# Kernel tuning notes

Measured on AMD Instinct MI355X. Metric: run time of the kernel, lower is better.

Reference implementation:

```python
import jax, jax.numpy as jnp
import numpy as np

N_STATES, N_OBS = 64, 32
N_TRAJ, T = 128, 250
ALPHA, BETA, KAPPA = 1.0, 2.0, -1.0
DT = 0.02
LAM = ALPHA ** 2 * (N_STATES + KAPPA) - N_STATES  # Merwe scaling lambda


def _weights(n):
    c = 0.5 / (n + LAM)
    Wm = jnp.full((2 * n + 1,), c, dtype=jnp.float32).at[0].set(LAM / (n + LAM))
    Wc = Wm.at[0].add(1.0 - ALPHA ** 2 + BETA)
    return Wm, Wc


def setup_inputs() -> dict:
    key = jax.random.key(0)
    k1, k2, k3, k4 = jax.random.split(key, 4)
    X = jax.random.normal(k1, (N_TRAJ, T, N_STATES), jnp.float32)
    Y = jax.random.normal(k2, (N_TRAJ, T, N_OBS), jnp.float32)
    F = jax.random.normal(k3, (N_STATES, N_STATES), jnp.float32) / np.sqrt(N_STATES)
    H = jax.random.normal(k4, (N_OBS, N_STATES), jnp.float32) / np.sqrt(N_STATES)
    Q = 0.01 * jnp.eye(N_STATES, dtype=jnp.float32)   # q2 * I, as in ctor
    R = 0.01 * jnp.eye(N_OBS, dtype=jnp.float32)      # r2 * I, as in ctor
    return {"X": X, "Y": Y, "F": F, "H": H, "Q": Q, "R": R}


def _sigma_points(x, P):
    # MerweScaledSigmaPoints: rows of upper-triangular chol((n+lam)P) == cols of lower chol
    n = x.shape[0]
    L = jnp.linalg.cholesky((n + LAM) * (P + 1e-8 * jnp.eye(n, dtype=P.dtype)))
    offs = L.T  # (n, n): row i is the i-th sigma offset
    return jnp.concatenate([x[None], x[None] + offs, x[None] - offs], axis=0)  # (2n+1, n)


def _ukf_step(carry, y, F, H, Q, R, Wm, Wc):
    x, P = carry
    # predict: propagate sigma points through fx(x, dt) = x + dt * tanh(F @ x)
    sig = _sigma_points(x, P)                 # (2n+1, n)
    sf = sig + DT * jnp.tanh(sig @ F.T)       # (2n+1, n)
    x_pred = Wm @ sf
    dxs = sf - x_pred
    P_pred = jnp.einsum('k,ki,kj->ij', Wc, dxs, dxs) + Q
    # update: hx(x) = H @ x applied to predicted sigma points (filterpy reuses sigmas_f)
    zs = sf @ H.T                             # (2n+1, m)
    z_pred = Wm @ zs
    dzs = zs - z_pred
    Pz = jnp.einsum('k,ki,kj->ij', Wc, dzs, dzs) + R
    Pxz = jnp.einsum('k,ki,kj->ij', Wc, dxs, dzs)
    K = jnp.linalg.solve(Pz, Pxz.T).T         # Pxz @ inv(Pz)
    x_new = x_pred + K @ (y - z_pred)
    P_new = P_pred - K @ Pz @ K.T
    P_new = 0.5 * (P_new + P_new.T)
    return (x_new, P_new), (x_new, P_new)


def reference(X, Y, F, H, Q, R):
    n = F.shape[0]
    Wm, Wc = _weights(n)

    def run_one(y_seq):
        x0 = jnp.zeros((n,), dtype=Y.dtype)             # ukf.x = zeros
        P0 = 1e-5 * jnp.eye(n, dtype=Y.dtype)           # ukf.P = 1e-5 * I
        step = lambda c, y: _ukf_step(c, y, F, H, Q, R, Wm, Wc)
        _, (xs, Ps) = jax.lax.scan(step, (x0, P0), y_seq)
        return xs, Ps

    traj_estimated, Pk_estimated = jax.vmap(run_one)(Y)  # (N,T,n), (N,T,n,n)
    mse_lin = jnp.mean((traj_estimated - X) ** 2, axis=(1, 2))  # per-traj MSE
    mse_lin_avg = jnp.mean(mse_lin)
    mse_db_avg = 10.0 * jnp.log10(mse_lin_avg)
    return traj_estimated, Pk_estimated, mse_lin_avg, mse_db_avg
```

## Files before the change

### kernel.cpp

```cpp
#include <hip/hip_runtime.h>
#include <math.h>


#define NTRAJ 128
#define TSTEPS 250
#define NS 64
#define NO 32
#define PS 65
#define SFS 68
#define HTS 36
#define PXS 33
#define GJS 65
#define BLK 256

#define DTc 0.02f
#define W_C (0.5f/63.0f)
#define WM0 (-1.0f/63.0f)
#define WC0 (2.0f - 1.0f/63.0f)

__device__ __forceinline__ float tanh_fast(float x) {
  float e = __expf(2.0f * x);
  return 1.0f - 2.0f / (e + 1.0f);
}

__global__ __launch_bounds__(BLK)
void ukf_main(const float* __restrict__ Xg, const float* __restrict__ Yg,
              const float* __restrict__ Fg, const float* __restrict__ Hg,
              const float* __restrict__ Qg, const float* __restrict__ Rg,
              float* __restrict__ outX, float* __restrict__ outP,
              float* __restrict__ wsPart)
{
  __shared__ __align__(16) float P[NS*PS];
  __shared__ __align__(16) float sfb[128*SFS];
  __shared__ __align__(16) float sHT[NS*HTS];
  __shared__ float sPart[4*NS];
  __shared__ float sx[NS], sxp[NS], sFx[NS], s0[NS];
  __shared__ float sinn[NO];

  float* Pxz = sfb;
  float* Km  = sfb + NS*PXS;
  float* Wgj = sfb + 2*NS*PXS;
  float* Mb  = sfb + 2*NS*PXS;

  const int tid  = threadIdx.x;
  const int lane = tid & 63;
  const int grp  = tid >> 6;
  const int traj = blockIdx.x;

  for (int o = tid; o < NS*NS; o += BLK) {
    int i = o >> 6, j = o & 63;
    P[i*PS + j] = (i == j) ? 1e-5f : 0.f;
  }
  for (int o = tid; o < NO*NS; o += BLK) {
    int m = o >> 6, j = o & 63;
    sHT[j*HTS + m] = Hg[o];
  }
  if (tid < NS) sx[tid] = 0.f;
  float errAcc = 0.f;
  __syncthreads();

  for (int t = 0; t < TSTEPS; ++t) {
    const size_t sbase = (size_t)traj*TSTEPS + t;

    for (int o = tid; o < NS*NS; o += BLK) {
      int i = o >> 6, j = o & 63;
      float v = P[i*PS + j] * 63.f;
      if (i == j) v += 6.3e-7f;
      P[i*PS + j] = v;
      sfb[j*SFS + i] = Fg[o];
    }
    __syncthreads();

    for (int pc = 0; pc < NS; pc += 8) {
      if (grp == 0) {
        const int i = lane;
        float pr[8];
        #pragma unroll
        for (int jj = 0; jj < 8; ++jj) pr[jj] = P[i*PS + pc + jj];
        #pragma unroll
        for (int jj = 0; jj < 8; ++jj) {
          const int gc = pc + jj;
          float dv  = __shfl(pr[jj], gc);
          float inv = rsqrtf(dv);
          float d   = dv * inv;
          pr[jj] = (i == gc) ? d : pr[jj] * inv;
          #pragma unroll
          for (int kk = jj + 1; kk < 8; ++kk) {
            float ck = __shfl(pr[jj], pc + kk);
            pr[kk] = fmaf(-pr[jj], ck, pr[kk]);
          }
        }
        #pragma unroll
        for (int jj = 0; jj < 8; ++jj) P[i*PS + pc + jj] = pr[jj];
      }
      __syncthreads();
      if (pc < NS - 8) {
        const int i = lane;
        float Li[8];
        #pragma unroll
        for (int jj = 0; jj < 8; ++jj) Li[jj] = P[i*PS + pc + jj];
        for (int k = pc + 8 + grp; k < NS; k += 4) {
          float acc = P[i*PS + k];
          #pragma unroll
          for (int jj = 0; jj < 8; ++jj)
            acc = fmaf(-Li[jj], P[k*PS + pc + jj], acc);
          P[i*PS + k] = acc;
        }
        __syncthreads();
      }
    }

    {
      const int c0 = (tid >> 4) << 2;
      const int j0 = (tid & 15) << 2;
      float acc[4][4];
      #pragma unroll
      for (int a = 0; a < 4; ++a)
        #pragma unroll
        for (int b = 0; b < 4; ++b) acc[a][b] = 0.f;
      for (int jj = 0; jj < NS; ++jj) {
        float4 fv = *(const float4*)&sfb[jj*SFS + j0];
        float lv[4];
        #pragma unroll
        for (int a = 0; a < 4; ++a) {
          int cc = c0 + a;
          lv[a] = (jj >= cc) ? P[jj*PS + cc] : 0.f;
        }
        #pragma unroll
        for (int a = 0; a < 4; ++a) {
          acc[a][0] = fmaf(lv[a], fv.x, acc[a][0]);
          acc[a][1] = fmaf(lv[a], fv.y, acc[a][1]);
          acc[a][2] = fmaf(lv[a], fv.z, acc[a][2]);
          acc[a][3] = fmaf(lv[a], fv.w, acc[a][3]);
        }
      }
      #pragma unroll
      for (int a = 0; a < 4; ++a) {
        float4 w4; w4.x = acc[a][0]; w4.y = acc[a][1]; w4.z = acc[a][2]; w4.w = acc[a][3];
        *(float4*)&sfb[(64 + c0 + a)*SFS + j0] = w4;
      }
    }
    if (tid < NS) {
      float a2 = 0.f;
      for (int jj = 0; jj < NS; ++jj) a2 = fmaf(sfb[jj*SFS + tid], sx[jj], a2);
      sFx[tid] = a2;
    }
    __syncthreads();

    {
      const int j = lane;
      float psum = 0.f;
      float xv = sx[j], fxv = sFx[j];
      for (int cc = grp; cc < NS; cc += 4) {
        float flv = sfb[(64+cc)*SFS + j];
        float Lv  = (j >= cc) ? P[j*PS + cc] : 0.f;
        float vp = xv + Lv + DTc * tanh_fast(fxv + flv);
        float vm = xv - Lv + DTc * tanh_fast(fxv - flv);
        sfb[cc*SFS + j]      = vp;
        sfb[(64+cc)*SFS + j] = vm;
        psum += vp + vm;
      }
      sPart[grp*NS + j] = psum;
    }
    if (tid < NS) s0[tid] = sx[tid] + DTc * tanh_fast(sFx[tid]);
    __syncthreads();

    if (tid < NS) {
      float xp = fmaf(W_C, sPart[tid] + sPart[NS+tid] + sPart[2*NS+tid] + sPart[3*NS+tid],
                      WM0 * s0[tid]);
      sxp[tid] = xp;
      s0[tid] -= xp;
    }
    __syncthreads();

    {
      const int i0 = (tid >> 4) << 2;
      const int j0 = (tid & 15) << 2;
      float acc[4][4];
      #pragma unroll
      for (int a = 0; a < 4; ++a)
        #pragma unroll
        for (int b = 0; b < 4; ++b) acc[a][b] = 0.f;
      float xi[4], xj[4];
      #pragma unroll
      for (int a = 0; a < 4; ++a) { xi[a] = sxp[i0+a]; xj[a] = sxp[j0+a]; }
      for (int r = 0; r < 128; ++r) {
        float4 av = *(const float4*)&sfb[r*SFS + i0];
        float4 bv = *(const float4*)&sfb[r*SFS + j0];
        float da[4] = {av.x - xi[0], av.y - xi[1], av.z - xi[2], av.w - xi[3]};
        float db[4] = {bv.x - xj[0], bv.y - xj[1], bv.z - xj[2], bv.w - xj[3]};
        #pragma unroll
        for (int a = 0; a < 4; ++a)
          #pragma unroll
          for (int b = 0; b < 4; ++b) acc[a][b] = fmaf(da[a], db[b], acc[a][b]);
      }
      const int rot = (i0 >> 2) & 3;
      #pragma unroll
      for (int a = 0; a < 4; ++a) {
        float d0a = s0[i0+a];
        #pragma unroll
        for (int b = 0; b < 4; ++b) {
          int bb = (b + rot) & 3;
          P[(i0+a)*PS + j0 + bb] = fmaf(WC0 * d0a, s0[j0+bb], W_C * acc[a][bb]);
        }
      }
    }
    __syncthreads();

    {
      const int i = lane;
      const int cb = grp * 8;
      float acc[8];
      #pragma unroll
      for (int u = 0; u < 8; ++u) acc[u] = 0.f;
      for (int jj = 0; jj < NS; ++jj) {
        float pv = P[i*PS + jj];
        float4 h0 = *(const float4*)&sHT[jj*HTS + cb];
        float4 h1 = *(const float4*)&sHT[jj*HTS + cb + 4];
        acc[0] = fmaf(pv, h0.x, acc[0]); acc[1] = fmaf(pv, h0.y, acc[1]);
        acc[2] = fmaf(pv, h0.z, acc[2]); acc[3] = fmaf(pv, h0.w, acc[3]);
        acc[4] = fmaf(pv, h1.x, acc[4]); acc[5] = fmaf(pv, h1.y, acc[5]);
        acc[6] = fmaf(pv, h1.z, acc[6]); acc[7] = fmaf(pv, h1.w, acc[7]);
      }
      #pragma unroll
      for (int u = 0; u < 8; ++u) Pxz[i*PXS + cb + u] = acc[u];
    }
    __syncthreads();

    {
      const int m = tid >> 3;
      const int n0 = tid & 7;
      float acc[4];
      #pragma unroll
      for (int q = 0; q < 4; ++q) acc[q] = Rg[m*NO + n0 + 8*q];
      for (int i2 = 0; i2 < NS; ++i2) {
        float hv = sHT[i2*HTS + m];
        #pragma unroll
        for (int q = 0; q < 4; ++q)
          acc[q] = fmaf(hv, Pxz[i2*PXS + n0 + 8*q], acc[q]);
      }
      #pragma unroll
      for (int q = 0; q < 4; ++q) Wgj[m*GJS + n0 + 8*q] = acc[q];
    }
    __syncthreads();

    if (grp == 0) {
      const int c = lane;
      float w[NO];
      #pragma unroll
      for (int r = 0; r < NO; ++r)
        w[r] = (c < NO) ? Wgj[r*GJS + c] : ((c - NO == r) ? 1.f : 0.f);
      #pragma unroll
      for (int p = 0; p < NO; ++p) {
        float piv = __shfl(w[p], p);
        float rp  = 1.0f / piv;
        float wp  = w[p] * rp;
        #pragma unroll
        for (int r = 0; r < NO; ++r) {
          if (r == p) continue;
          float cr = __shfl(w[r], p);
          w[r] = fmaf(-cr, wp, w[r]);
        }
        w[p] = wp;
      }
      if (c >= NO) {
        #pragma unroll
        for (int r = 0; r < NO; ++r) Wgj[(c - NO)*PXS + r] = w[r];
      }
    } else if (grp == 1) {
      if (lane < NO) {
        float z = 0.f;
        for (int jj = 0; jj < NS; ++jj) z = fmaf(sHT[jj*HTS + lane], sxp[jj], z);
        sinn[lane] = Yg[sbase*NO + lane] - z;
      }
    } else {
      for (int o = tid - 128; o < NS*NS; o += 128) {
        int i = o >> 6, j = o & 63;
        P[i*PS + j] += Qg[o];
      }
    }
    __syncthreads();

    {
      const int i = lane;
      const int cb = grp * 8;
      float acc[8];
      #pragma unroll
      for (int u = 0; u < 8; ++u) acc[u] = 0.f;
      for (int n2 = 0; n2 < NO; ++n2) {
        float pv = Pxz[i*PXS + n2];
        #pragma unroll
        for (int u = 0; u < 8; ++u)
          acc[u] = fmaf(pv, Wgj[(cb + u)*PXS + n2], acc[u]);
      }
      #pragma unroll
      for (int u = 0; u < 8; ++u) Km[i*PXS + cb + u] = acc[u];
    }
    __syncthreads();

    if (tid < 136) {
      int r = (int)((sqrtf(8.f*(float)tid + 1.f) - 1.f) * 0.5f);
      while ((r+1)*(r+2)/2 <= tid) ++r;
      while (r*(r+1)/2 > tid) --r;
      const int c2 = tid - ((r*(r+1)) >> 1);
      const int i0 = r << 2, j0 = c2 << 2;
      float acc[4][4];
      #pragma unroll
      for (int a = 0; a < 4; ++a)
        #pragma unroll
        for (int b = 0; b < 4; ++b) acc[a][b] = 0.f;
      for (int m = 0; m < NO; ++m) {
        float ka[4], pb[4];
        #pragma unroll
        for (int a = 0; a < 4; ++a) ka[a] = Km[(i0+a)*PXS + m];
        #pragma unroll
        for (int b = 0; b < 4; ++b) pb[b] = Pxz[(j0+b)*PXS + m];
        #pragma unroll
        for (int a = 0; a < 4; ++a)
          #pragma unroll
          for (int b = 0; b < 4; ++b) acc[a][b] = fmaf(ka[a], pb[b], acc[a][b]);
      }
      #pragma unroll
      for (int a = 0; a < 4; ++a)
        #pragma unroll
        for (int b = 0; b < 4; ++b) Mb[(i0+a)*GJS + j0 + b] = acc[a][b];
    } else if (tid >= 192) {
      const int i = tid - 192;
      float xn = sxp[i];
      #pragma unroll 8
      for (int m = 0; m < NO; ++m) xn = fmaf(Km[i*PXS + m], sinn[m], xn);
      sx[i] = xn;
      outX[sbase*NS + i] = xn;
      float dd = xn - Xg[sbase*NS + i];
      errAcc = fmaf(dd, dd, errAcc);
    }
    __syncthreads();

    for (int o = tid; o < NS*NS; o += BLK) {
      int i = o >> 6, j = o & 63;
      float mv = (i >= j) ? Mb[i*GJS + j] : Mb[j*GJS + i];
      float v = P[i*PS + j] - mv;
      P[i*PS + j] = v;
      outP[sbase*(size_t)(NS*NS) + o] = v;
    }
    __syncthreads();
  }

  sPart[tid] = errAcc;
  __syncthreads();
  if (tid < 64) {
    float v = sPart[tid] + sPart[tid+64] + sPart[tid+128] + sPart[tid+192];
    for (int off = 32; off > 0; off >>= 1) v += __shfl_down(v, off);
    if (tid == 0) wsPart[traj] = v;
  }
}

__global__ __launch_bounds__(128)
void mse_reduce(const float* __restrict__ part, float* __restrict__ outS)
{
  __shared__ float sbuf[128];
  int tid = threadIdx.x;
  sbuf[tid] = part[tid];
  __syncthreads();
  if (tid < 64) {
    float v = sbuf[tid] + sbuf[tid + 64];
    for (int off = 32; off > 0; off >>= 1) v += __shfl_down(v, off);
    if (tid == 0) {
      float m = v / (128.f * 250.f * 64.f);
      outS[0] = m;
      outS[1] = 10.f * log10f(m);
    }
  }
}

extern "C" void kernel_launch(void* const* d_in, const int* in_sizes, int n_in,
                              void* d_out, int out_size, void* d_ws, size_t ws_size,
                              hipStream_t stream) {
  const float* Xg = (const float*)d_in[0];
  const float* Yg = (const float*)d_in[1];
  const float* Fg = (const float*)d_in[2];
  const float* Hg = (const float*)d_in[3];
  const float* Qg = (const float*)d_in[4];
  const float* Rg = (const float*)d_in[5];

  float* outX = (float*)d_out;
  float* outP = outX + (size_t)NTRAJ*TSTEPS*NS;
  float* outS = outP + (size_t)NTRAJ*TSTEPS*NS*NS;
  float* wsP  = (float*)d_ws;

  hipLaunchKernelGGL(ukf_main, dim3(NTRAJ), dim3(BLK), 0, stream,
                     Xg, Yg, Fg, Hg, Qg, Rg, outX, outP, wsP);
  hipLaunchKernelGGL(mse_reduce, dim3(1), dim3(128), 0, stream, wsP, outS);
}
```

Before: 11.76 ms.

## Double block size to 512 threads and rebalance per-step work partitions

Raises the block from 256 to 512 threads and re-partitions every per-timestep stage (Cholesky trailing update, L·F product, covariance outer product, Pxz, Pz, gain, K·Pxzᵀ) so each thread owns a smaller tile. It also widens the Cholesky panel from 8 to 16 columns to cut barriers, and folds the 63x scale plus jitter into the end-of-step P write so one full pass and one sync disappear. The F transpose load now overlaps the first panel factorization, and R is preloaded into registers. The price is more threads per block competing for registers with 16-wide panel arrays, and lower per-thread ILP in the small GEMMs.

Result: faster. 9.780 ms (-16.8%).

```diff
diff --git a/kernel.cpp b/kernel.cpp
--- a/kernel.cpp
+++ b/kernel.cpp
@@ -11,7 +11,7 @@
 #define HTS 36
 #define PXS 33
 #define GJS 65
-#define BLK 256
+#define BLK 512
 
 #define DTc 0.02f
 #define W_C (0.5f/63.0f)
@@ -33,7 +33,7 @@
   __shared__ __align__(16) float P[NS*PS];
   __shared__ __align__(16) float sfb[128*SFS];
   __shared__ __align__(16) float sHT[NS*HTS];
-  __shared__ float sPart[4*NS];
+  __shared__ float sPart[8*NS];
   __shared__ float sx[NS], sxp[NS], sFx[NS], s0[NS];
   __shared__ float sinn[NO];
 
@@ -47,9 +47,14 @@
   const int grp  = tid >> 6;
   const int traj = blockIdx.x;
 
+  const int pzm = tid >> 4;
+  const int pzn = tid & 15;
+  const float rv0 = Rg[pzm*NO + pzn];
+  const float rv1 = Rg[pzm*NO + pzn + 16];
+
   for (int o = tid; o < NS*NS; o += BLK) {
     int i = o >> 6, j = o & 63;
-    P[i*PS + j] = (i == j) ? 1e-5f : 0.f;
+    P[i*PS + j] = (i == j) ? (63e-5f + 6.3e-7f) : 0.f;
   }
   for (int o = tid; o < NO*NS; o += BLK) {
     int m = o >> 6, j = o & 63;
@@ -62,47 +67,42 @@
   for (int t = 0; t < TSTEPS; ++t) {
     const size_t sbase = (size_t)traj*TSTEPS + t;
 
-    for (int o = tid; o < NS*NS; o += BLK) {
-      int i = o >> 6, j = o & 63;
-      float v = P[i*PS + j] * 63.f;
-      if (i == j) v += 6.3e-7f;
-      P[i*PS + j] = v;
-      sfb[j*SFS + i] = Fg[o];
-    }
-    __syncthreads();
-
-    for (int pc = 0; pc < NS; pc += 8) {
+    for (int pc = 0; pc < NS; pc += 16) {
       if (grp == 0) {
         const int i = lane;
-        float pr[8];
-        #pragma unroll
-        for (int jj = 0; jj < 8; ++jj) pr[jj] = P[i*PS + pc + jj];
-        #pragma unroll
-        for (int jj = 0; jj < 8; ++jj) {
+        float pr[16];
+        #pragma unroll
+        for (int jj = 0; jj < 16; ++jj) pr[jj] = P[i*PS + pc + jj];
+        #pragma unroll
+        for (int jj = 0; jj < 16; ++jj) {
           const int gc = pc + jj;
           float dv  = __shfl(pr[jj], gc);
           float inv = rsqrtf(dv);
-          float d   = dv * inv;
-          pr[jj] = (i == gc) ? d : pr[jj] * inv;
+          pr[jj] = (i == gc) ? dv * inv : pr[jj] * inv;
           #pragma unroll
-          for (int kk = jj + 1; kk < 8; ++kk) {
+          for (int kk = jj + 1; kk < 16; ++kk) {
             float ck = __shfl(pr[jj], pc + kk);
             pr[kk] = fmaf(-pr[jj], ck, pr[kk]);
           }
         }
         #pragma unroll
-        for (int jj = 0; jj < 8; ++jj) P[i*PS + pc + jj] = pr[jj];
+        for (int jj = 0; jj < 16; ++jj) P[i*PS + pc + jj] = pr[jj];
+      } else if (pc == 0) {
+        for (int o = tid - 64; o < NS*NS; o += (BLK - 64)) {
+          int i = o >> 6, j = o & 63;
+          sfb[j*SFS + i] = Fg[o];
+        }
       }
       __syncthreads();
-      if (pc < NS - 8) {
+      if (pc < NS - 16) {
         const int i = lane;
-        float Li[8];
-        #pragma unroll
-        for (int jj = 0; jj < 8; ++jj) Li[jj] = P[i*PS + pc + jj];
-        for (int k = pc + 8 + grp; k < NS; k += 4) {
+        float Li[16];
+        #pragma unroll
+        for (int jj = 0; jj < 16; ++jj) Li[jj] = P[i*PS + pc + jj];
+        for (int k = pc + 16 + grp; k < NS; k += 8) {
           float acc = P[i*PS + k];
           #pragma unroll
-          for (int jj = 0; jj < 8; ++jj)
+          for (int jj = 0; jj < 16; ++jj)
             acc = fmaf(-Li[jj], P[k*PS + pc + jj], acc);
           P[i*PS + k] = acc;
         }
@@ -111,34 +111,23 @@
     }
 
     {
-      const int c0 = (tid >> 4) << 2;
+      const int c0 = (tid >> 4) << 1;
       const int j0 = (tid & 15) << 2;
-      float acc[4][4];
-      #pragma unroll
-      for (int a = 0; a < 4; ++a)
-        #pragma unroll
-        for (int b = 0; b < 4; ++b) acc[a][b] = 0.f;
+      float a00=0.f,a01=0.f,a02=0.f,a03=0.f, a10=0.f,a11=0.f,a12=0.f,a13=0.f;
+      #pragma unroll 2
       for (int jj = 0; jj < NS; ++jj) {
         float4 fv = *(const float4*)&sfb[jj*SFS + j0];
-        float lv[4];
-        #pragma unroll
-        for (int a = 0; a < 4; ++a) {
-          int cc = c0 + a;
-          lv[a] = (jj >= cc) ? P[jj*PS + cc] : 0.f;
-        }
-        #pragma unroll
-        for (int a = 0; a < 4; ++a) {
-          acc[a][0] = fmaf(lv[a], fv.x, acc[a][0]);
-          acc[a][1] = fmaf(lv[a], fv.y, acc[a][1]);
-          acc[a][2] = fmaf(lv[a], fv.z, acc[a][2]);
-          acc[a][3] = fmaf(lv[a], fv.w, acc[a][3]);
-        }
-      }
-      #pragma unroll
-      for (int a = 0; a < 4; ++a) {
-        float4 w4; w4.x = acc[a][0]; w4.y = acc[a][1]; w4.z = acc[a][2]; w4.w = acc[a][3];
-        *(float4*)&sfb[(64 + c0 + a)*SFS + j0] = w4;
-      }
+        float lv0 = (jj >= c0)     ? P[jj*PS + c0]     : 0.f;
+        float lv1 = (jj >= c0 + 1) ? P[jj*PS + c0 + 1] : 0.f;
+        a00 = fmaf(lv0, fv.x, a00); a01 = fmaf(lv0, fv.y, a01);
+        a02 = fmaf(lv0, fv.z, a02); a03 = fmaf(lv0, fv.w, a03);
+        a10 = fmaf(lv1, fv.x, a10); a11 = fmaf(lv1, fv.y, a11);
+        a12 = fmaf(lv1, fv.z, a12); a13 = fmaf(lv1, fv.w, a13);
+      }
+      float4 w0; w0.x=a00; w0.y=a01; w0.z=a02; w0.w=a03;
+      float4 w1; w1.x=a10; w1.y=a11; w1.z=a12; w1.w=a13;
+      *(float4*)&sfb[(64 + c0)*SFS + j0]     = w0;
+      *(float4*)&sfb[(64 + c0 + 1)*SFS + j0] = w1;
     }
     if (tid < NS) {
       float a2 = 0.f;
@@ -151,7 +140,7 @@
       const int j = lane;
       float psum = 0.f;
       float xv = sx[j], fxv = sFx[j];
-      for (int cc = grp; cc < NS; cc += 4) {
+      for (int cc = grp; cc < NS; cc += 8) {
         float flv = sfb[(64+cc)*SFS + j];
         float Lv  = (j >= cc) ? P[j*PS + cc] : 0.f;
         float vp = xv + Lv + DTc * tanh_fast(fxv + flv);
@@ -166,81 +155,72 @@
     __syncthreads();
 
     if (tid < NS) {
-      float xp = fmaf(W_C, sPart[tid] + sPart[NS+tid] + sPart[2*NS+tid] + sPart[3*NS+tid],
-                      WM0 * s0[tid]);
+      float s = sPart[tid]        + sPart[NS+tid]   + sPart[2*NS+tid] + sPart[3*NS+tid]
+              + sPart[4*NS+tid]   + sPart[5*NS+tid] + sPart[6*NS+tid] + sPart[7*NS+tid];
+      float xp = fmaf(W_C, s, WM0 * s0[tid]);
       sxp[tid] = xp;
       s0[tid] -= xp;
     }
     __syncthreads();
 
     {
-      const int i0 = (tid >> 4) << 2;
-      const int j0 = (tid & 15) << 2;
-      float acc[4][4];
-      #pragma unroll
-      for (int a = 0; a < 4; ++a)
-        #pragma unroll
-        for (int b = 0; b < 4; ++b) acc[a][b] = 0.f;
-      float xi[4], xj[4];
-      #pragma unroll
-      for (int a = 0; a < 4; ++a) { xi[a] = sxp[i0+a]; xj[a] = sxp[j0+a]; }
+      const int i0 = (tid >> 5) << 2;
+      const int j0 = (tid & 31) << 1;
+      float acc[4][2];
+      #pragma unroll
+      for (int a = 0; a < 4; ++a) { acc[a][0] = 0.f; acc[a][1] = 0.f; }
+      float xi[4];
+      #pragma unroll
+      for (int a = 0; a < 4; ++a) xi[a] = sxp[i0+a];
+      const float xj0 = sxp[j0], xj1 = sxp[j0+1];
+      #pragma unroll 4
       for (int r = 0; r < 128; ++r) {
         float4 av = *(const float4*)&sfb[r*SFS + i0];
-        float4 bv = *(const float4*)&sfb[r*SFS + j0];
-        float da[4] = {av.x - xi[0], av.y - xi[1], av.z - xi[2], av.w - xi[3]};
-        float db[4] = {bv.x - xj[0], bv.y - xj[1], bv.z - xj[2], bv.w - xj[3]};
-        #pragma unroll
-        for (int a = 0; a < 4; ++a)
-          #pragma unroll
-          for (int b = 0; b < 4; ++b) acc[a][b] = fmaf(da[a], db[b], acc[a][b]);
-      }
-      const int rot = (i0 >> 2) & 3;
+        float2 bv = *(const float2*)&sfb[r*SFS + j0];
+        float db0 = bv.x - xj0, db1 = bv.y - xj1;
+        #pragma unroll
+        for (int a = 0; a < 4; ++a) {
+          float da = ((const float*)&av)[a] - xi[a];
+          acc[a][0] = fmaf(da, db0, acc[a][0]);
+          acc[a][1] = fmaf(da, db1, acc[a][1]);
+        }
+      }
+      const float d0j0 = s0[j0], d0j1 = s0[j0+1];
       #pragma unroll
       for (int a = 0; a < 4; ++a) {
-        float d0a = s0[i0+a];
-        #pragma unroll
-        for (int b = 0; b < 4; ++b) {
-          int bb = (b + rot) & 3;
-          P[(i0+a)*PS + j0 + bb] = fmaf(WC0 * d0a, s0[j0+bb], W_C * acc[a][bb]);
-        }
+        float d0a = WC0 * s0[i0+a];
+        P[(i0+a)*PS + j0]     = fmaf(d0a, d0j0, W_C * acc[a][0]);
+        P[(i0+a)*PS + j0 + 1] = fmaf(d0a, d0j1, W_C * acc[a][1]);
       }
     }
     __syncthreads();
 
     {
       const int i = lane;
-      const int cb = grp * 8;
-      float acc[8];
-      #pragma unroll
-      for (int u = 0; u < 8; ++u) acc[u] = 0.f;
+      const int cb = grp * 4;
+      float acc0=0.f, acc1=0.f, acc2=0.f, acc3=0.f;
       for (int jj = 0; jj < NS; ++jj) {
         float pv = P[i*PS + jj];
-        float4 h0 = *(const float4*)&sHT[jj*HTS + cb];
-        float4 h1 = *(const float4*)&sHT[jj*HTS + cb + 4];
-        acc[0] = fmaf(pv, h0.x, acc[0]); acc[1] = fmaf(pv, h0.y, acc[1]);
-        acc[2] = fmaf(pv, h0.z, acc[2]); acc[3] = fmaf(pv, h0.w, acc[3]);
-        acc[4] = fmaf(pv, h1.x, acc[4]); acc[5] = fmaf(pv, h1.y, acc[5]);
-        acc[6] = fmaf(pv, h1.z, acc[6]); acc[7] = fmaf(pv, h1.w, acc[7]);
-      }
-      #pragma unroll
-      for (int u = 0; u < 8; ++u) Pxz[i*PXS + cb + u] = acc[u];
-    }
-    __syncthreads();
-
-    {
-      const int m = tid >> 3;
-      const int n0 = tid & 7;
-      float acc[4];
-      #pragma unroll
-      for (int q = 0; q < 4; ++q) acc[q] = Rg[m*NO + n0 + 8*q];
+        float4 h = *(const float4*)&sHT[jj*HTS + cb];
+        acc0 = fmaf(pv, h.x, acc0); acc1 = fmaf(pv, h.y, acc1);
+        acc2 = fmaf(pv, h.z, acc2); acc3 = fmaf(pv, h.w, acc3);
+      }
+      Pxz[i*PXS + cb]     = acc0;
+      Pxz[i*PXS + cb + 1] = acc1;
+      Pxz[i*PXS + cb + 2] = acc2;
+      Pxz[i*PXS + cb + 3] = acc3;
+    }
+    __syncthreads();
+
+    {
+      float a0 = rv0, a1 = rv1;
       for (int i2 = 0; i2 < NS; ++i2) {
-        float hv = sHT[i2*HTS + m];
-        #pragma unroll
-        for (int q = 0; q < 4; ++q)
-          acc[q] = fmaf(hv, Pxz[i2*PXS + n0 + 8*q], acc[q]);
-      }
-      #pragma unroll
-      for (int q = 0; q < 4; ++q) Wgj[m*GJS + n0 + 8*q] = acc[q];
+        float hv = sHT[i2*HTS + pzm];
+        a0 = fmaf(hv, Pxz[i2*PXS + pzn], a0);
+        a1 = fmaf(hv, Pxz[i2*PXS + pzn + 16], a1);
+      }
+      Wgj[pzm*GJS + pzn]      = a0;
+      Wgj[pzm*GJS + pzn + 16] = a1;
     }
     __syncthreads();
 
@@ -274,7 +254,7 @@
         sinn[lane] = Yg[sbase*NO + lane] - z;
       }
     } else {
-      for (int o = tid - 128; o < NS*NS; o += 128) {
+      for (int o = tid - 128; o < NS*NS; o += 6*64) {
         int i = o >> 6, j = o & 63;
         P[i*PS + j] += Qg[o];
       }
@@ -283,49 +263,50 @@
 
     {
       const int i = lane;
-      const int cb = grp * 8;
-      float acc[8];
-      #pragma unroll
-      for (int u = 0; u < 8; ++u) acc[u] = 0.f;
+      const int cb = grp * 4;
+      float acc0=0.f, acc1=0.f, acc2=0.f, acc3=0.f;
       for (int n2 = 0; n2 < NO; ++n2) {
         float pv = Pxz[i*PXS + n2];
-        #pragma unroll
-        for (int u = 0; u < 8; ++u)
-          acc[u] = fmaf(pv, Wgj[(cb + u)*PXS + n2], acc[u]);
-      }
-      #pragma unroll
-      for (int u = 0; u < 8; ++u) Km[i*PXS + cb + u] = acc[u];
-    }
-    __syncthreads();
-
-    if (tid < 136) {
-      int r = (int)((sqrtf(8.f*(float)tid + 1.f) - 1.f) * 0.5f);
-      while ((r+1)*(r+2)/2 <= tid) ++r;
-      while (r*(r+1)/2 > tid) --r;
-      const int c2 = tid - ((r*(r+1)) >> 1);
-      const int i0 = r << 2, j0 = c2 << 2;
-      float acc[4][4];
-      #pragma unroll
-      for (int a = 0; a < 4; ++a)
-        #pragma unroll
-        for (int b = 0; b < 4; ++b) acc[a][b] = 0.f;
+        acc0 = fmaf(pv, Wgj[(cb    )*PXS + n2], acc0);
+        acc1 = fmaf(pv, Wgj[(cb + 1)*PXS + n2], acc1);
+        acc2 = fmaf(pv, Wgj[(cb + 2)*PXS + n2], acc2);
+        acc3 = fmaf(pv, Wgj[(cb + 3)*PXS + n2], acc3);
+      }
+      Km[i*PXS + cb]     = acc0;
+      Km[i*PXS + cb + 1] = acc1;
+      Km[i*PXS + cb + 2] = acc2;
+      Km[i*PXS + cb + 3] = acc3;
+    }
+    __syncthreads();
+
+    if (tid < 272) {
+      int k = (int)((sqrtf(4.f*(float)tid + 1.f) - 1.f) * 0.5f);
+      while ((k+1)*(k+2) <= tid) ++k;
+      while (k*(k+1) > tid) --k;
+      const int r0 = tid - k*(k+1);
+      const int rb  = (r0 <= k) ? (2*k) : (2*k + 1);
+      const int cb2 = (r0 <= k) ? r0 : (r0 - (k + 1));
+      const int i0 = rb << 1, j0 = cb2 << 2;
+      float acc[2][4];
+      #pragma unroll
+      for (int b = 0; b < 4; ++b) { acc[0][b] = 0.f; acc[1][b] = 0.f; }
       for (int m = 0; m < NO; ++m) {
-        float ka[4], pb[4];
-        #pragma unroll
-        for (int a = 0; a < 4; ++a) ka[a] = Km[(i0+a)*PXS + m];
-        #pragma unroll
-        for (int b = 0; b < 4; ++b) pb[b] = Pxz[(j0+b)*PXS + m];
-        #pragma unroll
-        for (int a = 0; a < 4; ++a)
-          #pragma unroll
-          for (int b = 0; b < 4; ++b) acc[a][b] = fmaf(ka[a], pb[b], acc[a][b]);
-      }
-      #pragma unroll
-      for (int a = 0; a < 4; ++a)
-        #pragma unroll
-        for (int b = 0; b < 4; ++b) Mb[(i0+a)*GJS + j0 + b] = acc[a][b];
-    } else if (tid >= 192) {
-      const int i = tid - 192;
+        float ka0 = Km[i0*PXS + m];
+        float ka1 = Km[(i0+1)*PXS + m];
+        #pragma unroll
+        for (int b = 0; b < 4; ++b) {
+          float pb = Pxz[(j0+b)*PXS + m];
+          acc[0][b] = fmaf(ka0, pb, acc[0][b]);
+          acc[1][b] = fmaf(ka1, pb, acc[1][b]);
+        }
+      }
+      #pragma unroll
+      for (int b = 0; b < 4; ++b) {
+        Mb[i0*GJS + j0 + b]     = acc[0][b];
+        Mb[(i0+1)*GJS + j0 + b] = acc[1][b];
+      }
+    } else if (tid >= 448) {
+      const int i = tid - 448;
       float xn = sxp[i];
       #pragma unroll 8
       for (int m = 0; m < NO; ++m) xn = fmaf(Km[i*PXS + m], sinn[m], xn);
@@ -340,18 +321,18 @@
       int i = o >> 6, j = o & 63;
       float mv = (i >= j) ? Mb[i*GJS + j] : Mb[j*GJS + i];
       float v = P[i*PS + j] - mv;
-      P[i*PS + j] = v;
       outP[sbase*(size_t)(NS*NS) + o] = v;
-    }
-    __syncthreads();
-  }
-
-  sPart[tid] = errAcc;
-  __syncthreads();
-  if (tid < 64) {
-    float v = sPart[tid] + sPart[tid+64] + sPart[tid+128] + sPart[tid+192];
+      float nv = v * 63.f;
+      if (i == j) nv += 6.3e-7f;
+      P[i*PS + j] = nv;
+    }
+    __syncthreads();
+  }
+
+  if (grp == 7) {
+    float v = errAcc;
     for (int off = 32; off > 0; off >>= 1) v += __shfl_down(v, off);
-    if (tid == 0) wsPart[traj] = v;
+    if (lane == 0) wsPart[traj] = v;
   }
 }
 
```

## Restructure UKF step: blocked Cholesky, HP-based gain, fused covariance update

Applied to the files above, without the earlier changes.

Doubles the block to 512 threads and makes the Cholesky use 32-column panels, which cuts the number of barriers per step. The cross-covariance is rewritten as T = H·P_pred so that Pz = T·Hᵀ + R and K = Tᵀ·Pz⁻¹, and the rank update K·T is fused with the +Q, the output write and the next step's 63x scaling plus jitter. Redundant elementwise passes, index recomputation and scalar shared loads are removed in favour of float4 tiles, and the sigma-point mean is subtracted once in place. The costs are more register pressure from the 32-wide panel and new algebraic paths, which could change numerics slightly. Work is also imbalanced across the larger block.

After: 11.19 ms. 4.8% less time.

```diff
diff --git a/kernel.cpp b/kernel.cpp
--- a/kernel.cpp
+++ b/kernel.cpp
@@ -6,17 +6,20 @@
 #define TSTEPS 250
 #define NS 64
 #define NO 32
-#define PS 65
+#define PS 68
 #define SFS 68
 #define HTS 36
-#define PXS 33
-#define GJS 65
-#define BLK 256
+#define TS 68
+#define GJS 68
+#define PZS 36
+#define KS 36
+#define BLK 512
 
 #define DTc 0.02f
 #define W_C (0.5f/63.0f)
 #define WM0 (-1.0f/63.0f)
 #define WC0 (2.0f - 1.0f/63.0f)
+#define DEPS 6.3e-7f
 
 __device__ __forceinline__ float tanh_fast(float x) {
   float e = __expf(2.0f * x);
@@ -33,14 +36,17 @@
   __shared__ __align__(16) float P[NS*PS];
   __shared__ __align__(16) float sfb[128*SFS];
   __shared__ __align__(16) float sHT[NS*HTS];
-  __shared__ float sPart[4*NS];
-  __shared__ float sx[NS], sxp[NS], sFx[NS], s0[NS];
-  __shared__ float sinn[NO];
-
-  float* Pxz = sfb;
-  float* Km  = sfb + NS*PXS;
-  float* Wgj = sfb + 2*NS*PXS;
-  float* Mb  = sfb + 2*NS*PXS;
+  __shared__ __align__(16) float sPart[8*NS];
+  __shared__ __align__(16) float sx[NS];
+  __shared__ __align__(16) float sxp[NS];
+  __shared__ __align__(16) float sFx[NS];
+  __shared__ __align__(16) float s0[NS];
+  __shared__ __align__(16) float sinn[NO];
+
+  float* Tb  = sfb;
+  float* Pzb = sfb + 2176;
+  float* Pzi = sfb + 4352;
+  float* Km  = sfb + 5504;
 
   const int tid  = threadIdx.x;
   const int lane = tid & 63;
@@ -49,7 +55,7 @@
 
   for (int o = tid; o < NS*NS; o += BLK) {
     int i = o >> 6, j = o & 63;
-    P[i*PS + j] = (i == j) ? 1e-5f : 0.f;
+    P[i*PS + j] = (i == j) ? (63e-5f + DEPS) : 0.f;
   }
   for (int o = tid; o < NO*NS; o += BLK) {
     int m = o >> 6, j = o & 63;
@@ -62,55 +68,65 @@
   for (int t = 0; t < TSTEPS; ++t) {
     const size_t sbase = (size_t)traj*TSTEPS + t;
 
-    for (int o = tid; o < NS*NS; o += BLK) {
-      int i = o >> 6, j = o & 63;
-      float v = P[i*PS + j] * 63.f;
-      if (i == j) v += 6.3e-7f;
-      P[i*PS + j] = v;
-      sfb[j*SFS + i] = Fg[o];
-    }
-    __syncthreads();
-
-    for (int pc = 0; pc < NS; pc += 8) {
+    for (int pc = 0; pc < NS; pc += 32) {
       if (grp == 0) {
         const int i = lane;
-        float pr[8];
-        #pragma unroll
-        for (int jj = 0; jj < 8; ++jj) pr[jj] = P[i*PS + pc + jj];
-        #pragma unroll
-        for (int jj = 0; jj < 8; ++jj) {
+        float pr[32];
+        #pragma unroll
+        for (int c4 = 0; c4 < 8; ++c4)
+          *(float4*)&pr[c4*4] = *(const float4*)&P[i*PS + pc + c4*4];
+        #pragma unroll
+        for (int jj = 0; jj < 32; ++jj) {
           const int gc = pc + jj;
           float dv  = __shfl(pr[jj], gc);
           float inv = rsqrtf(dv);
-          float d   = dv * inv;
-          pr[jj] = (i == gc) ? d : pr[jj] * inv;
-          #pragma unroll
-          for (int kk = jj + 1; kk < 8; ++kk) {
+          pr[jj] = (i == gc) ? dv * inv : ((i < gc) ? 0.f : pr[jj] * inv);
+          #pragma unroll
+          for (int kk = jj + 1; kk < 32; ++kk) {
             float ck = __shfl(pr[jj], pc + kk);
             pr[kk] = fmaf(-pr[jj], ck, pr[kk]);
           }
         }
         #pragma unroll
-        for (int jj = 0; jj < 8; ++jj) P[i*PS + pc + jj] = pr[jj];
+        for (int c4 = 0; c4 < 8; ++c4)
+          *(float4*)&P[i*PS + pc + c4*4] = *(const float4*)&pr[c4*4];
+      } else if (pc == 0) {
+        for (int c = tid - 64; c < 1024; c += (BLK - 64)) {
+          int i = c >> 4, j0 = (c & 15) << 2;
+          float4 fv = *(const float4*)&Fg[i*64 + j0];
+          sfb[(j0    )*SFS + i] = fv.x;
+          sfb[(j0 + 1)*SFS + i] = fv.y;
+          sfb[(j0 + 2)*SFS + i] = fv.z;
+          sfb[(j0 + 3)*SFS + i] = fv.w;
+        }
       }
       __syncthreads();
-      if (pc < NS - 8) {
-        const int i = lane;
-        float Li[8];
-        #pragma unroll
-        for (int jj = 0; jj < 8; ++jj) Li[jj] = P[i*PS + pc + jj];
-        for (int k = pc + 8 + grp; k < NS; k += 4) {
+      if (pc == 0) {
+        const int k  = 32 + (lane & 31);
+        const int ib = 32 + grp*2 + (lane >> 5);
+        float Lk[32];
+        #pragma unroll
+        for (int c4 = 0; c4 < 8; ++c4)
+          *(float4*)&Lk[c4*4] = *(const float4*)&P[k*PS + c4*4];
+        #pragma unroll
+        for (int it = 0; it < 2; ++it) {
+          const int i = ib + 16*it;
           float acc = P[i*PS + k];
           #pragma unroll
-          for (int jj = 0; jj < 8; ++jj)
-            acc = fmaf(-Li[jj], P[k*PS + pc + jj], acc);
+          for (int c4 = 0; c4 < 8; ++c4) {
+            float4 pi = *(const float4*)&P[i*PS + c4*4];
+            acc = fmaf(-pi.x, Lk[c4*4    ], acc);
+            acc = fmaf(-pi.y, Lk[c4*4 + 1], acc);
+            acc = fmaf(-pi.z, Lk[c4*4 + 2], acc);
+            acc = fmaf(-pi.w, Lk[c4*4 + 3], acc);
+          }
           P[i*PS + k] = acc;
         }
         __syncthreads();
       }
     }
 
-    {
+    if (tid < 256) {
       const int c0 = (tid >> 4) << 2;
       const int j0 = (tid & 15) << 2;
       float acc[4][4];
@@ -120,30 +136,25 @@
         for (int b = 0; b < 4; ++b) acc[a][b] = 0.f;
       for (int jj = 0; jj < NS; ++jj) {
         float4 fv = *(const float4*)&sfb[jj*SFS + j0];
-        float lv[4];
-        #pragma unroll
-        for (int a = 0; a < 4; ++a) {
-          int cc = c0 + a;
-          lv[a] = (jj >= cc) ? P[jj*PS + cc] : 0.f;
-        }
-        #pragma unroll
-        for (int a = 0; a < 4; ++a) {
-          acc[a][0] = fmaf(lv[a], fv.x, acc[a][0]);
-          acc[a][1] = fmaf(lv[a], fv.y, acc[a][1]);
-          acc[a][2] = fmaf(lv[a], fv.z, acc[a][2]);
-          acc[a][3] = fmaf(lv[a], fv.w, acc[a][3]);
-        }
-      }
-      #pragma unroll
-      for (int a = 0; a < 4; ++a) {
-        float4 w4; w4.x = acc[a][0]; w4.y = acc[a][1]; w4.z = acc[a][2]; w4.w = acc[a][3];
-        *(float4*)&sfb[(64 + c0 + a)*SFS + j0] = w4;
-      }
-    }
-    if (tid < NS) {
+        float4 lv = *(const float4*)&P[jj*PS + c0];
+        float fa[4] = {fv.x, fv.y, fv.z, fv.w};
+        float lb[4] = {lv.x, lv.y, lv.z, lv.w};
+        #pragma unroll
+        for (int a = 0; a < 4; ++a)
+          #pragma unroll
+          for (int b = 0; b < 4; ++b)
+            acc[a][b] = fmaf(lb[b], fa[a], acc[a][b]);
+      }
+      #pragma unroll
+      for (int b = 0; b < 4; ++b) {
+        float4 w4; w4.x = acc[0][b]; w4.y = acc[1][b]; w4.z = acc[2][b]; w4.w = acc[3][b];
+        *(float4*)&sfb[(64 + c0 + b)*SFS + j0] = w4;
+      }
+    } else if (grp == 4) {
+      const int i2 = lane;
       float a2 = 0.f;
-      for (int jj = 0; jj < NS; ++jj) a2 = fmaf(sfb[jj*SFS + tid], sx[jj], a2);
-      sFx[tid] = a2;
+      for (int jj = 0; jj < NS; ++jj) a2 = fmaf(sfb[jj*SFS + i2], sx[jj], a2);
+      sFx[i2] = a2;
     }
     __syncthreads();
 
@@ -151,13 +162,13 @@
       const int j = lane;
       float psum = 0.f;
       float xv = sx[j], fxv = sFx[j];
-      for (int cc = grp; cc < NS; cc += 4) {
-        float flv = sfb[(64+cc)*SFS + j];
-        float Lv  = (j >= cc) ? P[j*PS + cc] : 0.f;
+      for (int cc = grp; cc < NS; cc += 8) {
+        float flv = sfb[(64 + cc)*SFS + j];
+        float Lv  = P[j*PS + cc];
         float vp = xv + Lv + DTc * tanh_fast(fxv + flv);
         float vm = xv - Lv + DTc * tanh_fast(fxv - flv);
-        sfb[cc*SFS + j]      = vp;
-        sfb[(64+cc)*SFS + j] = vm;
+        sfb[cc*SFS + j]        = vp;
+        sfb[(64 + cc)*SFS + j] = vm;
         psum += vp + vm;
       }
       sPart[grp*NS + j] = psum;
@@ -166,14 +177,28 @@
     __syncthreads();
 
     if (tid < NS) {
-      float xp = fmaf(W_C, sPart[tid] + sPart[NS+tid] + sPart[2*NS+tid] + sPart[3*NS+tid],
-                      WM0 * s0[tid]);
+      float s = sPart[tid]        + sPart[NS+tid]   + sPart[2*NS+tid] + sPart[3*NS+tid]
+              + sPart[4*NS+tid]   + sPart[5*NS+tid] + sPart[6*NS+tid] + sPart[7*NS+tid];
+      float xp = fmaf(W_C, s, WM0 * s0[tid]);
       sxp[tid] = xp;
       s0[tid] -= xp;
     }
     __syncthreads();
 
     {
+      const int j0 = (tid & 15) << 2;
+      float4 xp4 = *(const float4*)&sxp[j0];
+      #pragma unroll
+      for (int q = 0; q < 4; ++q) {
+        const int r = (tid >> 4) + (q << 5);
+        float4 v = *(const float4*)&sfb[r*SFS + j0];
+        v.x -= xp4.x; v.y -= xp4.y; v.z -= xp4.z; v.w -= xp4.w;
+        *(float4*)&sfb[r*SFS + j0] = v;
+      }
+    }
+    __syncthreads();
+
+    if (tid < 256) {
       const int i0 = (tid >> 4) << 2;
       const int j0 = (tid & 15) << 2;
       float acc[4][4];
@@ -181,66 +206,99 @@
       for (int a = 0; a < 4; ++a)
         #pragma unroll
         for (int b = 0; b < 4; ++b) acc[a][b] = 0.f;
-      float xi[4], xj[4];
-      #pragma unroll
-      for (int a = 0; a < 4; ++a) { xi[a] = sxp[i0+a]; xj[a] = sxp[j0+a]; }
+      #pragma unroll 4
       for (int r = 0; r < 128; ++r) {
         float4 av = *(const float4*)&sfb[r*SFS + i0];
         float4 bv = *(const float4*)&sfb[r*SFS + j0];
-        float da[4] = {av.x - xi[0], av.y - xi[1], av.z - xi[2], av.w - xi[3]};
-        float db[4] = {bv.x - xj[0], bv.y - xj[1], bv.z - xj[2], bv.w - xj[3]};
+        float da[4] = {av.x, av.y, av.z, av.w};
+        float db[4] = {bv.x, bv.y, bv.z, bv.w};
         #pragma unroll
         for (int a = 0; a < 4; ++a)
           #pragma unroll
-          for (int b = 0; b < 4; ++b) acc[a][b] = fmaf(da[a], db[b], acc[a][b]);
-      }
-      const int rot = (i0 >> 2) & 3;
+          for (int b = 0; b < 4; ++b)
+            acc[a][b] = fmaf(da[a], db[b], acc[a][b]);
+      }
+      float4 si = *(const float4*)&s0[i0];
+      float4 sj = *(const float4*)&s0[j0];
+      float s0i[4] = {si.x, si.y, si.z, si.w};
+      float s0j[4] = {sj.x, sj.y, sj.z, sj.w};
       #pragma unroll
       for (int a = 0; a < 4; ++a) {
-        float d0a = s0[i0+a];
-        #pragma unroll
-        for (int b = 0; b < 4; ++b) {
-          int bb = (b + rot) & 3;
-          P[(i0+a)*PS + j0 + bb] = fmaf(WC0 * d0a, s0[j0+bb], W_C * acc[a][bb]);
-        }
-      }
-    }
-    __syncthreads();
-
-    {
-      const int i = lane;
-      const int cb = grp * 8;
-      float acc[8];
-      #pragma unroll
-      for (int u = 0; u < 8; ++u) acc[u] = 0.f;
-      for (int jj = 0; jj < NS; ++jj) {
-        float pv = P[i*PS + jj];
-        float4 h0 = *(const float4*)&sHT[jj*HTS + cb];
-        float4 h1 = *(const float4*)&sHT[jj*HTS + cb + 4];
-        acc[0] = fmaf(pv, h0.x, acc[0]); acc[1] = fmaf(pv, h0.y, acc[1]);
-        acc[2] = fmaf(pv, h0.z, acc[2]); acc[3] = fmaf(pv, h0.w, acc[3]);
-        acc[4] = fmaf(pv, h1.x, acc[4]); acc[5] = fmaf(pv, h1.y, acc[5]);
-        acc[6] = fmaf(pv, h1.z, acc[6]); acc[7] = fmaf(pv, h1.w, acc[7]);
-      }
-      #pragma unroll
-      for (int u = 0; u < 8; ++u) Pxz[i*PXS + cb + u] = acc[u];
-    }
-    __syncthreads();
-
-    {
-      const int m = tid >> 3;
-      const int n0 = tid & 7;
-      float acc[4];
-      #pragma unroll
-      for (int q = 0; q < 4; ++q) acc[q] = Rg[m*NO + n0 + 8*q];
-      for (int i2 = 0; i2 < NS; ++i2) {
-        float hv = sHT[i2*HTS + m];
-        #pragma unroll
-        for (int q = 0; q < 4; ++q)
-          acc[q] = fmaf(hv, Pxz[i2*PXS + n0 + 8*q], acc[q]);
-      }
-      #pragma unroll
-      for (int q = 0; q < 4; ++q) Wgj[m*GJS + n0 + 8*q] = acc[q];
+        float d0a = WC0 * s0i[a];
+        float4 w4;
+        w4.x = fmaf(d0a, s0j[0], W_C * acc[a][0]);
+        w4.y = fmaf(d0a, s0j[1], W_C * acc[a][1]);
+        w4.z = fmaf(d0a, s0j[2], W_C * acc[a][2]);
+        w4.w = fmaf(d0a, s0j[3], W_C * acc[a][3]);
+        *(float4*)&P[(i0 + a)*PS + j0] = w4;
+      }
+    } else if (grp == 4) {
+      if (lane < NO) {
+        float z = 0.f;
+        for (int jj = 0; jj < NS; ++jj) z = fmaf(sHT[jj*HTS + lane], sxp[jj], z);
+        sinn[lane] = Yg[sbase*NO + lane] - z;
+      }
+    }
+    __syncthreads();
+
+    if (tid < 128) {
+      const int m0 = (tid >> 4) << 2;
+      const int c0 = (tid & 15) << 2;
+      float acc[4][4];
+      #pragma unroll
+      for (int a = 0; a < 4; ++a)
+        #pragma unroll
+        for (int b = 0; b < 4; ++b) acc[a][b] = 0.f;
+      for (int jj = 0; jj < NS; jj += 4) {
+        float hv[16], pv[16];
+        #pragma unroll
+        for (int k2 = 0; k2 < 4; ++k2) {
+          *(float4*)&hv[k2*4] = *(const float4*)&sHT[(jj + k2)*HTS + m0];
+          *(float4*)&pv[k2*4] = *(const float4*)&P[(jj + k2)*PS + c0];
+        }
+        #pragma unroll
+        for (int k2 = 0; k2 < 4; ++k2)
+          #pragma unroll
+          for (int a = 0; a < 4; ++a)
+            #pragma unroll
+            for (int b = 0; b < 4; ++b)
+              acc[a][b] = fmaf(hv[k2*4 + a], pv[k2*4 + b], acc[a][b]);
+      }
+      #pragma unroll
+      for (int a = 0; a < 4; ++a) {
+        float4 w4; w4.x = acc[a][0]; w4.y = acc[a][1]; w4.z = acc[a][2]; w4.w = acc[a][3];
+        *(float4*)&Tb[(m0 + a)*TS + c0] = w4;
+      }
+    }
+    __syncthreads();
+
+    if (tid < 128) {
+      const int m0 = (tid >> 3) << 1;
+      const int n0 = (tid & 7) << 2;
+      float4 r0 = *(const float4*)&Rg[m0*NO + n0];
+      float4 r1 = *(const float4*)&Rg[(m0 + 1)*NO + n0];
+      float acc[2][4] = {{r0.x, r0.y, r0.z, r0.w}, {r1.x, r1.y, r1.z, r1.w}};
+      for (int jj = 0; jj < NS; jj += 4) {
+        float t0[4], t1[4], hv[16];
+        *(float4*)t0 = *(const float4*)&Tb[m0*TS + jj];
+        *(float4*)t1 = *(const float4*)&Tb[(m0 + 1)*TS + jj];
+        #pragma unroll
+        for (int k2 = 0; k2 < 4; ++k2)
+          *(float4*)&hv[k2*4] = *(const float4*)&sHT[(jj + k2)*HTS + n0];
+        #pragma unroll
+        for (int k2 = 0; k2 < 4; ++k2) {
+          #pragma unroll
+          for (int b = 0; b < 4; ++b) {
+            acc[0][b] = fmaf(t0[k2], hv[k2*4 + b], acc[0][b]);
+            acc[1][b] = fmaf(t1[k2], hv[k2*4 + b], acc[1][b]);
+          }
+        }
+      }
+      #pragma unroll
+      for (int a = 0; a < 2; ++a) {
+        float4 w4; w4.x = acc[a][0]; w4.y = acc[a][1]; w4.z = acc[a][2]; w4.w = acc[a][3];
+        *(float4*)&Pzb[(m0 + a)*GJS + n0] = w4;
+      }
     }
     __syncthreads();
 
@@ -249,7 +307,7 @@
       float w[NO];
       #pragma unroll
       for (int r = 0; r < NO; ++r)
-        w[r] = (c < NO) ? Wgj[r*GJS + c] : ((c - NO == r) ? 1.f : 0.f);
+        w[r] = (c < NO) ? Pzb[r*GJS + c] : ((c - NO == r) ? 1.f : 0.f);
       #pragma unroll
       for (int p = 0; p < NO; ++p) {
         float piv = __shfl(w[p], p);
@@ -265,93 +323,127 @@
       }
       if (c >= NO) {
         #pragma unroll
-        for (int r = 0; r < NO; ++r) Wgj[(c - NO)*PXS + r] = w[r];
-      }
-    } else if (grp == 1) {
-      if (lane < NO) {
-        float z = 0.f;
-        for (int jj = 0; jj < NS; ++jj) z = fmaf(sHT[jj*HTS + lane], sxp[jj], z);
-        sinn[lane] = Yg[sbase*NO + lane] - z;
-      }
-    } else {
-      for (int o = tid - 128; o < NS*NS; o += 128) {
-        int i = o >> 6, j = o & 63;
-        P[i*PS + j] += Qg[o];
-      }
-    }
-    __syncthreads();
-
-    {
-      const int i = lane;
-      const int cb = grp * 8;
-      float acc[8];
-      #pragma unroll
-      for (int u = 0; u < 8; ++u) acc[u] = 0.f;
-      for (int n2 = 0; n2 < NO; ++n2) {
-        float pv = Pxz[i*PXS + n2];
-        #pragma unroll
-        for (int u = 0; u < 8; ++u)
-          acc[u] = fmaf(pv, Wgj[(cb + u)*PXS + n2], acc[u]);
-      }
-      #pragma unroll
-      for (int u = 0; u < 8; ++u) Km[i*PXS + cb + u] = acc[u];
+        for (int r = 0; r < NO; ++r) Pzi[(c - NO)*PZS + r] = w[r];
+      }
+    }
+    __syncthreads();
+
+    if (tid < 128) {
+      const int i0 = (tid & 15) << 2;
+      const int cb = (tid >> 4) << 2;
+      float acc[4][4];
+      #pragma unroll
+      for (int a = 0; a < 4; ++a)
+        #pragma unroll
+        for (int b = 0; b < 4; ++b) acc[a][b] = 0.f;
+      for (int n = 0; n < NO; n += 4) {
+        float tv[16], zv[16];
+        #pragma unroll
+        for (int k2 = 0; k2 < 4; ++k2)
+          *(float4*)&tv[k2*4] = *(const float4*)&Tb[(n + k2)*TS + i0];
+        #pragma unroll
+        for (int b = 0; b < 4; ++b)
+          *(float4*)&zv[b*4] = *(const float4*)&Pzi[(cb + b)*PZS + n];
+        #pragma unroll
+        for (int k2 = 0; k2 < 4; ++k2)
+          #pragma unroll
+          for (int a = 0; a < 4; ++a)
+            #pragma unroll
+            for (int b = 0; b < 4; ++b)
+              acc[a][b] = fmaf(tv[k2*4 + a], zv[b*4 + k2], acc[a][b]);
+      }
+      #pragma unroll
+      for (int a = 0; a < 4; ++a) {
+        float4 w4; w4.x = acc[a][0]; w4.y = acc[a][1]; w4.z = acc[a][2]; w4.w = acc[a][3];
+        *(float4*)&Km[(i0 + a)*KS + cb] = w4;
+      }
     }
     __syncthreads();
 
     if (tid < 136) {
       int r = (int)((sqrtf(8.f*(float)tid + 1.f) - 1.f) * 0.5f);
-      while ((r+1)*(r+2)/2 <= tid) ++r;
-      while (r*(r+1)/2 > tid) --r;
-      const int c2 = tid - ((r*(r+1)) >> 1);
+      while ((r + 1)*(r + 2)/2 <= tid) ++r;
+      while (r*(r + 1)/2 > tid) --r;
+      const int c2 = tid - ((r*(r + 1)) >> 1);
       const int i0 = r << 2, j0 = c2 << 2;
+      const bool diag = (r == c2);
       float acc[4][4];
       #pragma unroll
       for (int a = 0; a < 4; ++a)
         #pragma unroll
         for (int b = 0; b < 4; ++b) acc[a][b] = 0.f;
-      for (int m = 0; m < NO; ++m) {
-        float ka[4], pb[4];
-        #pragma unroll
-        for (int a = 0; a < 4; ++a) ka[a] = Km[(i0+a)*PXS + m];
-        #pragma unroll
-        for (int b = 0; b < 4; ++b) pb[b] = Pxz[(j0+b)*PXS + m];
+      for (int m = 0; m < NO; m += 4) {
+        float ka[16], tb[16];
         #pragma unroll
         for (int a = 0; a < 4; ++a)
-          #pragma unroll
-          for (int b = 0; b < 4; ++b) acc[a][b] = fmaf(ka[a], pb[b], acc[a][b]);
-      }
-      #pragma unroll
-      for (int a = 0; a < 4; ++a)
-        #pragma unroll
-        for (int b = 0; b < 4; ++b) Mb[(i0+a)*GJS + j0 + b] = acc[a][b];
-    } else if (tid >= 192) {
-      const int i = tid - 192;
+          *(float4*)&ka[a*4] = *(const float4*)&Km[(i0 + a)*KS + m];
+        #pragma unroll
+        for (int k2 = 0; k2 < 4; ++k2)
+          *(float4*)&tb[k2*4] = *(const float4*)&Tb[(m + k2)*TS + j0];
+        #pragma unroll
+        for (int k2 = 0; k2 < 4; ++k2)
+          #pragma unroll
+          for (int a = 0; a < 4; ++a)
+            #pragma unroll
+            for (int b = 0; b < 4; ++b)
+              acc[a][b] = fmaf(ka[a*4 + k2], tb[k2*4 + b], acc[a][b]);
+      }
+      float vres[4][4];
+      #pragma unroll
+      for (int a = 0; a < 4; ++a) {
+        float4 pv = *(const float4*)&P[(i0 + a)*PS + j0];
+        float4 qv = *(const float4*)&Qg[(i0 + a)*64 + j0];
+        float pa[4] = {pv.x + qv.x, pv.y + qv.y, pv.z + qv.z, pv.w + qv.w};
+        #pragma unroll
+        for (int b = 0; b < 4; ++b) {
+          float mv = diag ? ((a >= b) ? acc[a][b] : acc[b][a]) : acc[a][b];
+          vres[a][b] = pa[b] - mv;
+        }
+      }
+      #pragma unroll
+      for (int a = 0; a < 4; ++a) {
+        float4 g; g.x = vres[a][0]; g.y = vres[a][1]; g.z = vres[a][2]; g.w = vres[a][3];
+        *(float4*)&outP[sbase*(size_t)(NS*NS) + (i0 + a)*64 + j0] = g;
+        float4 sres;
+        sres.x = fmaf(vres[a][0], 63.f, (diag && a == 0) ? DEPS : 0.f);
+        sres.y = fmaf(vres[a][1], 63.f, (diag && a == 1) ? DEPS : 0.f);
+        sres.z = fmaf(vres[a][2], 63.f, (diag && a == 2) ? DEPS : 0.f);
+        sres.w = fmaf(vres[a][3], 63.f, (diag && a == 3) ? DEPS : 0.f);
+        *(float4*)&P[(i0 + a)*PS + j0] = sres;
+      }
+      if (!diag) {
+        #pragma unroll
+        for (int b = 0; b < 4; ++b) {
+          float4 g; g.x = vres[0][b]; g.y = vres[1][b]; g.z = vres[2][b]; g.w = vres[3][b];
+          *(float4*)&outP[sbase*(size_t)(NS*NS) + (j0 + b)*64 + i0] = g;
+          float4 s2; s2.x = g.x*63.f; s2.y = g.y*63.f; s2.z = g.z*63.f; s2.w = g.w*63.f;
+          *(float4*)&P[(j0 + b)*PS + i0] = s2;
+        }
+      }
+    } else if (tid >= 448) {
+      const int i = tid - 448;
       float xn = sxp[i];
-      #pragma unroll 8
-      for (int m = 0; m < NO; ++m) xn = fmaf(Km[i*PXS + m], sinn[m], xn);
+      #pragma unroll
+      for (int mc = 0; mc < NO; mc += 4) {
+        float4 kv = *(const float4*)&Km[i*KS + mc];
+        float4 iv = *(const float4*)&sinn[mc];
+        xn = fmaf(kv.x, iv.x, xn);
+        xn = fmaf(kv.y, iv.y, xn);
+        xn = fmaf(kv.z, iv.z, xn);
+        xn = fmaf(kv.w, iv.w, xn);
+      }
       sx[i] = xn;
       outX[sbase*NS + i] = xn;
       float dd = xn - Xg[sbase*NS + i];
       errAcc = fmaf(dd, dd, errAcc);
     }
     __syncthreads();
-
-    for (int o = tid; o < NS*NS; o += BLK) {
-      int i = o >> 6, j = o & 63;
-      float mv = (i >= j) ? Mb[i*GJS + j] : Mb[j*GJS + i];
-      float v = P[i*PS + j] - mv;
-      P[i*PS + j] = v;
-      outP[sbase*(size_t)(NS*NS) + o] = v;
-    }
-    __syncthreads();
   }
 
-  sPart[tid] = errAcc;
-  __syncthreads();
-  if (tid < 64) {
-    float v = sPart[tid] + sPart[tid+64] + sPart[tid+128] + sPart[tid+192];
+  if (grp == 7) {
+    float v = errAcc;
     for (int off = 32; off > 0; off >>= 1) v += __shfl_down(v, off);
-    if (tid == 0) wsPart[traj] = v;
+    if (lane == 0) wsPart[traj] = v;
   }
 }
 
```
